# Kernel optimization log

Measured on AMD Instinct MI355X. Metric: run time of the kernel, lower is better.

## Reference

```python
import jax, jax.numpy as jnp
import numpy as np

N_CHANNELS = 512
D_K = 64
N_HEADS = N_CHANNELS // D_K  # 8
SCALE = 1.0 / np.sqrt(np.sqrt(D_K))
EPS = 1e-8


def pixnorm(x, axis=-1):
    return x * jax.lax.rsqrt(jnp.mean(x * x, axis=axis, keepdims=True) + EPS)


def setup_inputs() -> dict:
    key = jax.random.key(0)
    k1, k2, k3 = jax.random.split(key, 3)
    x = jax.random.normal(k1, (16, N_CHANNELS, 32, 32), dtype=jnp.float32)
    # 1x1 conv weights (bias=False) stored as [out, in]
    w_proj = jax.random.normal(k2, (3 * N_CHANNELS, N_CHANNELS), dtype=jnp.float32) * (1.0 / np.sqrt(N_CHANNELS))
    w_out = jax.random.normal(k3, (N_CHANNELS, N_CHANNELS), dtype=jnp.float32) * (1.0 / np.sqrt(N_CHANNELS))
    return {"x": x, "w_proj": w_proj, "w_out": w_out}


def reference(x, w_proj, w_out):
    B, C, H, W = x.shape
    S = H * W
    # tokens: [B, S, C]
    xt = x.reshape(B, C, S).transpose(0, 2, 1)
    # 1x1 conv projection -> [B, S, 3C]
    h = jnp.einsum('bsc,oc->bso', xt, w_proj)
    qkv = h.reshape(B, S, N_HEADS, 3 * D_K)
    q, k, v = jnp.split(qkv, 3, axis=-1)  # each [B, S, H, d]
    q = pixnorm(q)
    k = pixnorm(k)
    v = pixnorm(v)
    attn = jnp.einsum('bihd,bjhd->bijh', q * SCALE, k * SCALE)
    attn = jax.nn.softmax(attn, axis=2)
    res = jnp.einsum('bijh,bjhd->bihd', attn, v)  # [B, S, H, d]
    res = res.reshape(B, S, C)
    res = jnp.einsum('bsc,oc->bso', res, w_out)
    res = res.transpose(0, 2, 1).reshape(B, C, H, W)
    return x + res
```

## Files before the change

### kernel.cpp

```cpp
#include <hip/hip_runtime.h>
#include <hip/hip_bf16.h>
#include <math.h>

typedef float f32x4 __attribute__((ext_vector_type(4)));
typedef __bf16 bf16x8 __attribute__((ext_vector_type(8)));
typedef __bf16 bf16x4 __attribute__((ext_vector_type(4)));
typedef unsigned u32x4 __attribute__((ext_vector_type(4)));

#define DEVFN static __device__ __forceinline__

DEVFN void gload16(const void* g, void* l) {
  __builtin_amdgcn_global_load_lds(
      (const __attribute__((address_space(1))) unsigned int*)g,
      (__attribute__((address_space(3))) unsigned int*)l, 16, 0, 0);
}

DEVFN f32x4 mfma16(bf16x8 a, bf16x8 b, f32x4 c) {
  return __builtin_amdgcn_mfma_f32_16x16x32_bf16(a, b, c, 0, 0, 0);
}

DEVFN unsigned cvtpk(float lo, float hi) {
  unsigned r;
  asm("v_cvt_pk_bf16_f32 %0, %1, %2" : "=v"(r) : "v"(lo), "v"(hi));
  return r;
}

__global__ __launch_bounds__(256) void cast_weights_k(
    const float* __restrict__ wp, const float* __restrict__ wo,
    __bf16* __restrict__ wpb, __bf16* __restrict__ wob) {
  int i = blockIdx.x * 256 + threadIdx.x;
  if (i < 1536 * 512) {
    wpb[i] = (__bf16)wp[i];
  } else {
    int j = i - 1536 * 512;
    wob[j] = (__bf16)wo[j];
  }
}

__global__ __launch_bounds__(256) void transpose_x_k(const float* __restrict__ x,
                                                     __bf16* __restrict__ xt) {
  __shared__ float tile[64][65];
  int b = blockIdx.z, c0 = blockIdx.y * 64, s0 = blockIdx.x * 64;
  int t = threadIdx.x;
  int r = t >> 2, q = (t & 3) << 4;
  const float* src = x + ((size_t)(b * 512 + c0 + r)) * 1024 + s0 + q;
#pragma unroll
  for (int i = 0; i < 4; i++) {
    float4 f = *reinterpret_cast<const float4*>(src + i * 4);
    tile[r][q + i * 4 + 0] = f.x;
    tile[r][q + i * 4 + 1] = f.y;
    tile[r][q + i * 4 + 2] = f.z;
    tile[r][q + i * 4 + 3] = f.w;
  }
  __syncthreads();
  bf16x8 o0, o1;
#pragma unroll
  for (int i = 0; i < 8; i++) o0[i] = (__bf16)tile[q + i][r];
#pragma unroll
  for (int i = 0; i < 8; i++) o1[i] = (__bf16)tile[q + 8 + i][r];
  __bf16* dst = xt + ((size_t)(b * 1024 + s0 + r)) * 512 + c0 + q;
  *reinterpret_cast<bf16x8*>(dst) = o0;
  *reinterpret_cast<bf16x8*>(dst + 8) = o1;
}

template <int MODE>
__global__ __launch_bounds__(256) void gemm_bt_k(
    const __bf16* __restrict__ A, const __bf16* __restrict__ Bt,
    float* __restrict__ Cf, const float* __restrict__ Xres,
    __bf16* __restrict__ Qo, __bf16* __restrict__ Ko, __bf16* __restrict__ Vto,
    int ldc, long bstride_bt, long bstride_c) {
  __shared__ __attribute__((aligned(16))) char smem[32768];
  const int K = 512;
  int n0 = blockIdx.x * 128, m0 = blockIdx.y * 128;
  int z = blockIdx.z;
  Bt += (size_t)z * bstride_bt;
  int tid = threadIdx.x, wave = tid >> 6, lane = tid & 63;
  int fr = lane & 15, fq = lane >> 4;
  int wm = (wave >> 1) * 64, wn = (wave & 1) * 64;
  f32x4 acc[4][4] = {};
  int od[4], ro[4], sp[4];
#pragma unroll
  for (int i = 0; i < 4; i++) {
    od[i] = wave * 4096 + i * 1024 + lane * 16;
    ro[i] = od[i] >> 7;
    sp[i] = (od[i] & 127) ^ ((ro[i] & 7) << 4);
  }
  int rsw = (fr & 7) << 4;
  const char* Ap = (const char*)A;
  const char* Bp = (const char*)Bt;
  for (int k0 = 0; k0 < K; k0 += 64) {
    __syncthreads();
#pragma unroll
    for (int i = 0; i < 4; i++)
      gload16(Ap + (size_t)(m0 + ro[i]) * 1024 + k0 * 2 + sp[i], smem + od[i]);
#pragma unroll
    for (int i = 0; i < 4; i++)
      gload16(Bp + (size_t)(n0 + ro[i]) * 1024 + k0 * 2 + sp[i], smem + 16384 + od[i]);
    __syncthreads();
#pragma unroll
    for (int kk = 0; kk < 2; kk++) {
      bf16x8 af[4], bfr[4];
#pragma unroll
      for (int mi = 0; mi < 4; mi++)
        af[mi] = *reinterpret_cast<const bf16x8*>(
            smem + (wm + mi * 16 + fr) * 128 + ((kk * 64 + fq * 16) ^ rsw));
#pragma unroll
      for (int ni = 0; ni < 4; ni++)
        bfr[ni] = *reinterpret_cast<const bf16x8*>(
            smem + 16384 + (wn + ni * 16 + fr) * 128 + ((kk * 64 + fq * 16) ^ rsw));
      __builtin_amdgcn_s_setprio(1);
#pragma unroll
      for (int mi = 0; mi < 4; mi++)
#pragma unroll
        for (int ni = 0; ni < 4; ni++)
          acc[mi][ni] = mfma16(af[mi], bfr[ni], acc[mi][ni]);
      __builtin_amdgcn_s_setprio(0);
    }
  }
  if (MODE == 1) {
    float* Co = Cf + (size_t)z * bstride_c;
    const float* Xr = Xres + (size_t)z * bstride_c;
#pragma unroll
    for (int mi = 0; mi < 4; mi++)
#pragma unroll
      for (int i = 0; i < 4; i++) {
        int row = m0 + wm + mi * 16 + fq * 4 + i;
#pragma unroll
        for (int ni = 0; ni < 4; ni++) {
          size_t idx = (size_t)row * ldc + n0 + wn + ni * 16 + fr;
          Co[idx] = acc[mi][ni][i] + Xr[idx];
        }
      }
  } else {
    int g0 = n0 + wn;
    int head = g0 / 192;
    int grp = (g0 >> 6) % 3;
    int b = m0 >> 10, sb = m0 & 1023;
    int bh = b * 8 + head;
    float nrm[4][4];
#pragma unroll
    for (int mi = 0; mi < 4; mi++)
#pragma unroll
      for (int i = 0; i < 4; i++) {
        float ss = 0.f;
#pragma unroll
        for (int ni = 0; ni < 4; ni++) ss += acc[mi][ni][i] * acc[mi][ni][i];
#pragma unroll
        for (int off = 1; off < 16; off <<= 1) ss += __shfl_xor(ss, off);
        float nv = rsqrtf(ss * (1.0f / 64.0f) + 1e-8f);
        if (grp == 0) nv *= 0.18033688011112042f;
        nrm[mi][i] = nv;
      }
    if (grp < 2) {
      __bf16* dst = (grp == 0 ? Qo : Ko) + (size_t)bh * 65536;
#pragma unroll
      for (int mi = 0; mi < 4; mi++)
#pragma unroll
        for (int i = 0; i < 4; i++) {
          int s = sb + wm + mi * 16 + fq * 4 + i;
#pragma unroll
          for (int ni = 0; ni < 4; ni++)
            dst[(size_t)s * 64 + ni * 16 + fr] = (__bf16)(acc[mi][ni][i] * nrm[mi][i]);
        }
    }
    __syncthreads();
    if (grp == 2) {
#pragma unroll
      for (int mi = 0; mi < 4; mi++)
#pragma unroll
        for (int i = 0; i < 4; i++) {
          int r = wm + mi * 16 + fq * 4 + i;
#pragma unroll
          for (int ni = 0; ni < 4; ni++) {
            int col2 = (2 * (ni * 16 + fr)) ^ ((r & 31) << 2);
            *(__bf16*)(smem + r * 128 + col2) = (__bf16)(acc[mi][ni][i] * nrm[mi][i]);
          }
        }
    }
    __syncthreads();
    if (grp == 2) {
      int sl = wm + lane;
      int l = sl & 63;
      int pl = ((l >> 2) & 3) * 16 + (l >> 4) * 4 + (l & 3);
      __bf16* vdst = Vto + (size_t)bh * 65536 + sb + (sl & 64) + pl;
#pragma unroll 8
      for (int d = 0; d < 64; d++) {
        __bf16 v = *(const __bf16*)(smem + sl * 128 + ((2 * d) ^ ((sl & 31) << 2)));
        vdst[(size_t)d * 1024] = v;
      }
    }
  }
}

__global__ __launch_bounds__(256, 4) void attn_k(const __bf16* __restrict__ Q,
                                                 const __bf16* __restrict__ Kb,
                                                 const __bf16* __restrict__ Vt,
                                                 __bf16* __restrict__ Res) {
  __shared__ __attribute__((aligned(16))) char lds[32768];
  int p = blockIdx.x;
  int v = (p & 7) * 128 + (p >> 3);
  int qt = v & 7, bh = v >> 3;
  int wave = threadIdx.x >> 6, lane = threadIdx.x & 63;
  int fr = lane & 15, fq = lane >> 4;
  const __bf16* Qb = Q + (size_t)bh * 65536;
  const char* Kbase = (const char*)(Kb + (size_t)bh * 65536);
  const char* Vbase = (const char*)(Vt + (size_t)bh * 65536);
  bf16x8 qf[2][2];
#pragma unroll
  for (int qs = 0; qs < 2; qs++)
#pragma unroll
    for (int kk = 0; kk < 2; kk++)
      qf[qs][kk] = *reinterpret_cast<const bf16x8*>(
          Qb + (size_t)(qt * 128 + qs * 64 + wave * 16 + fr) * 64 + kk * 32 + fq * 8);

  bf16x8 ones;
#pragma unroll
  for (int j = 0; j < 8; j++) ones[j] = (__bf16)1.0f;

  f32x4 oa[2][4] = {};
  f32x4 lacc[2] = {};

  int o0 = wave * 2048 + lane * 16;
  int o1 = o0 + 1024;
  int r0 = o0 >> 7, c0 = o0 & 127, r1 = o1 >> 7, c1 = o1 & 127;
  int s0 = c0 ^ ((r0 & 7) << 4), s1 = c1 ^ ((r1 & 7) << 4);
  int swr = (fr & 7) << 4;

#define STAGE(kt_, buf_)                                                        \
  {                                                                             \
    char* ks_ = lds + (buf_)*8192;                                              \
    char* vs_ = lds + 16384 + (buf_)*8192;                                      \
    gload16(Kbase + (size_t)(kt_)*8192 + r0 * 128 + s0, ks_ + o0);              \
    gload16(Kbase + (size_t)(kt_)*8192 + r1 * 128 + s1, ks_ + o1);              \
    gload16(Vbase + (size_t)r0 * 2048 + (kt_)*128 + s0, vs_ + o0);              \
    gload16(Vbase + (size_t)r1 * 2048 + (kt_)*128 + s1, vs_ + o1);              \
  }

  STAGE(0, 0);
  __syncthreads();
  for (int kt = 0; kt < 16; kt++) {
    int cur = kt & 1;
    if (kt + 1 < 16) STAGE(kt + 1, cur ^ 1);
    const char* ksc = lds + cur * 8192;
    const char* vsc = lds + 16384 + cur * 8192;
    f32x4 sa[2][4] = {};
    __builtin_amdgcn_s_setprio(1);
#pragma unroll
    for (int ni = 0; ni < 4; ni++) {
      bf16x8 kf0 = *reinterpret_cast<const bf16x8*>(
          ksc + (ni * 16 + fr) * 128 + ((fq * 16) ^ swr));
      bf16x8 kf1 = *reinterpret_cast<const bf16x8*>(
          ksc + (ni * 16 + fr) * 128 + ((64 + fq * 16) ^ swr));
#pragma unroll
      for (int qs = 0; qs < 2; qs++) {
        sa[qs][ni] = mfma16(kf0, qf[qs][0], sa[qs][ni]);
        sa[qs][ni] = mfma16(kf1, qf[qs][1], sa[qs][ni]);
      }
    }
    __builtin_amdgcn_s_setprio(0);
    bf16x8 pb[2][2];
#pragma unroll
    for (int qs = 0; qs < 2; qs++) {
#pragma unroll
      for (int ni = 0; ni < 4; ni++)
#pragma unroll
        for (int i = 0; i < 4; i++)
          sa[qs][ni][i] = __builtin_amdgcn_exp2f(sa[qs][ni][i]);
#pragma unroll
      for (int kk2 = 0; kk2 < 2; kk2++) {
        u32x4 u;
        u[0] = cvtpk(sa[qs][2 * kk2][0], sa[qs][2 * kk2][1]);
        u[1] = cvtpk(sa[qs][2 * kk2][2], sa[qs][2 * kk2][3]);
        u[2] = cvtpk(sa[qs][2 * kk2 + 1][0], sa[qs][2 * kk2 + 1][1]);
        u[3] = cvtpk(sa[qs][2 * kk2 + 1][2], sa[qs][2 * kk2 + 1][3]);
        pb[qs][kk2] = __builtin_bit_cast(bf16x8, u);
      }
      lacc[qs] = mfma16(ones, pb[qs][0], lacc[qs]);
      lacc[qs] = mfma16(ones, pb[qs][1], lacc[qs]);
    }
    __builtin_amdgcn_s_setprio(1);
#pragma unroll
    for (int nd = 0; nd < 4; nd++) {
      int vrow = (nd * 16 + fr) * 128;
#pragma unroll
      for (int kk2 = 0; kk2 < 2; kk2++) {
        bf16x8 vf = *reinterpret_cast<const bf16x8*>(
            vsc + vrow + ((fq * 32 + kk2 * 16) ^ swr));
#pragma unroll
        for (int qs = 0; qs < 2; qs++)
          oa[qs][nd] = mfma16(vf, pb[qs][kk2], oa[qs][nd]);
      }
    }
    __builtin_amdgcn_s_setprio(0);
    __syncthreads();
  }
  int b = bh >> 3, hd = bh & 7;
#pragma unroll
  for (int qs = 0; qs < 2; qs++) {
    int q = qt * 128 + qs * 64 + wave * 16 + fr;
    float inv_l = 1.0f / lacc[qs][0];
    __bf16* dst = Res + ((size_t)(b * 1024 + q)) * 512 + hd * 64 + fq * 4;
#pragma unroll
    for (int nd = 0; nd < 4; nd++) {
      bf16x4 ov;
#pragma unroll
      for (int i = 0; i < 4; i++) ov[i] = (__bf16)(oa[qs][nd][i] * inv_l);
      *reinterpret_cast<bf16x4*>(dst + nd * 16) = ov;
    }
  }
#undef STAGE
}

extern "C" void kernel_launch(void* const* d_in, const int* in_sizes, int n_in,
                              void* d_out, int out_size, void* d_ws, size_t ws_size,
                              hipStream_t stream) {
  const float* x = (const float*)d_in[0];
  const float* wp = (const float*)d_in[1];
  const float* wo = (const float*)d_in[2];
  float* out = (float*)d_out;
  char* w = (char*)d_ws;
  __bf16* wpb = (__bf16*)(w);
  __bf16* wob = (__bf16*)(w + 1572864);
  __bf16* xt = (__bf16*)(w + 2097152);
  __bf16* Qb = (__bf16*)(w + 18874368);
  __bf16* Kb = (__bf16*)(w + 35651584);
  __bf16* Vtb = (__bf16*)(w + 52428800);
  __bf16* resb = (__bf16*)(w + 69206016);

  cast_weights_k<<<4096, 256, 0, stream>>>(wp, wo, wpb, wob);
  transpose_x_k<<<dim3(16, 8, 16), 256, 0, stream>>>(x, xt);
  gemm_bt_k<2><<<dim3(12, 128, 1), 256, 0, stream>>>(xt, wpb, nullptr, nullptr,
                                                     Qb, Kb, Vtb, 1536, 0, 0);
  attn_k<<<1024, 256, 0, stream>>>(Qb, Kb, Vtb, resb);
  gemm_bt_k<1><<<dim3(8, 4, 16), 256, 0, stream>>>(wob, resb, out, x,
                                                   nullptr, nullptr, nullptr, 1024,
                                                   1024L * 512, 512L * 1024);
}
```

Measured before the change: 123.9 us.

## Double-buffer GEMM LDS tiles and remap blocks for XCD-local L2 reuse

The projection and output GEMMs now use a two-stage LDS ring with a K-step of 32. The next tile's global-to-LDS loads are issued before the current tile's MFMAs, which leaves one barrier per iteration instead of two. Blocks move to a 1D grid with an XCD-aware mapping, so blocks on the same XCD share A rows (MODE 2) or batch slices (MODE 1) for better L2 locality. The smaller K-step doubles the iteration count, and the swizzle is reworked for 64-byte rows.

```diff
diff --git a/kernel.cpp b/kernel.cpp
--- a/kernel.cpp
+++ b/kernel.cpp
@@ -67,59 +67,80 @@
 __global__ __launch_bounds__(256) void gemm_bt_k(
     const __bf16* __restrict__ A, const __bf16* __restrict__ Bt,
     float* __restrict__ Cf, const float* __restrict__ Xres,
-    __bf16* __restrict__ Qo, __bf16* __restrict__ Ko, __bf16* __restrict__ Vto,
-    int ldc, long bstride_bt, long bstride_c) {
+    __bf16* __restrict__ Qo, __bf16* __restrict__ Ko, __bf16* __restrict__ Vto) {
   __shared__ __attribute__((aligned(16))) char smem[32768];
   const int K = 512;
-  int n0 = blockIdx.x * 128, m0 = blockIdx.y * 128;
-  int z = blockIdx.z;
-  Bt += (size_t)z * bstride_bt;
+  int p = blockIdx.x, xcd = p & 7, idx = p >> 3;
+  int m0, n0, z;
+  if (MODE == 2) {
+    m0 = (xcd * 16 + idx / 12) * 128;
+    n0 = (idx % 12) * 128;
+    z = 0;
+  } else {
+    z = xcd * 2 + idx / 32;
+    int rem = idx % 32;
+    m0 = (rem >> 3) * 128;
+    n0 = (rem & 7) * 128;
+    Bt += (size_t)z * (1024L * 512);
+  }
   int tid = threadIdx.x, wave = tid >> 6, lane = tid & 63;
   int fr = lane & 15, fq = lane >> 4;
   int wm = (wave >> 1) * 64, wn = (wave & 1) * 64;
   f32x4 acc[4][4] = {};
-  int od[4], ro[4], sp[4];
-#pragma unroll
-  for (int i = 0; i < 4; i++) {
-    od[i] = wave * 4096 + i * 1024 + lane * 16;
-    ro[i] = od[i] >> 7;
-    sp[i] = (od[i] & 127) ^ ((ro[i] & 7) << 4);
-  }
-  int rsw = (fr & 7) << 4;
+  int offs[2], rr[2], scc[2];
+#pragma unroll
+  for (int i = 0; i < 2; i++) {
+    offs[i] = wave * 2048 + i * 1024 + lane * 16;
+    rr[i] = offs[i] >> 6;
+    scc[i] = (offs[i] & 63) ^ (((rr[i] ^ (rr[i] >> 2)) & 3) << 4);
+  }
+  int rdsw = (fr ^ (fr >> 2)) & 3;
   const char* Ap = (const char*)A;
   const char* Bp = (const char*)Bt;
-  for (int k0 = 0; k0 < K; k0 += 64) {
+
+#define GSTAGE(k0_, buf_)                                                       \
+  {                                                                             \
+    char* as_ = smem + (buf_)*8192;                                             \
+    char* bs_ = smem + 16384 + (buf_)*8192;                                     \
+    _Pragma("unroll") for (int i = 0; i < 2; i++)                               \
+        gload16(Ap + (size_t)(m0 + rr[i]) * 1024 + (k0_)*2 + scc[i],            \
+                as_ + offs[i]);                                                 \
+    _Pragma("unroll") for (int i = 0; i < 2; i++)                               \
+        gload16(Bp + (size_t)(n0 + rr[i]) * 1024 + (k0_)*2 + scc[i],            \
+                bs_ + offs[i]);                                                 \
+  }
+
+  GSTAGE(0, 0);
+  __syncthreads();
+  int cur = 0;
+  for (int k0 = 0; k0 < K; k0 += 32) {
+    if (k0 + 32 < K) GSTAGE(k0 + 32, cur ^ 1);
+    const char* as = smem + cur * 8192;
+    const char* bs = smem + 16384 + cur * 8192;
+    bf16x8 af[4], bfr[4];
+#pragma unroll
+    for (int mi = 0; mi < 4; mi++)
+      af[mi] = *reinterpret_cast<const bf16x8*>(
+          as + (wm + mi * 16 + fr) * 64 + ((fq ^ rdsw) << 4));
+#pragma unroll
+    for (int ni = 0; ni < 4; ni++)
+      bfr[ni] = *reinterpret_cast<const bf16x8*>(
+          bs + (wn + ni * 16 + fr) * 64 + ((fq ^ rdsw) << 4));
+    __builtin_amdgcn_s_setprio(1);
+#pragma unroll
+    for (int mi = 0; mi < 4; mi++)
+#pragma unroll
+      for (int ni = 0; ni < 4; ni++)
+        acc[mi][ni] = mfma16(af[mi], bfr[ni], acc[mi][ni]);
+    __builtin_amdgcn_s_setprio(0);
     __syncthreads();
-#pragma unroll
-    for (int i = 0; i < 4; i++)
-      gload16(Ap + (size_t)(m0 + ro[i]) * 1024 + k0 * 2 + sp[i], smem + od[i]);
-#pragma unroll
-    for (int i = 0; i < 4; i++)
-      gload16(Bp + (size_t)(n0 + ro[i]) * 1024 + k0 * 2 + sp[i], smem + 16384 + od[i]);
-    __syncthreads();
-#pragma unroll
-    for (int kk = 0; kk < 2; kk++) {
-      bf16x8 af[4], bfr[4];
-#pragma unroll
-      for (int mi = 0; mi < 4; mi++)
-        af[mi] = *reinterpret_cast<const bf16x8*>(
-            smem + (wm + mi * 16 + fr) * 128 + ((kk * 64 + fq * 16) ^ rsw));
-#pragma unroll
-      for (int ni = 0; ni < 4; ni++)
-        bfr[ni] = *reinterpret_cast<const bf16x8*>(
-            smem + 16384 + (wn + ni * 16 + fr) * 128 + ((kk * 64 + fq * 16) ^ rsw));
-      __builtin_amdgcn_s_setprio(1);
-#pragma unroll
-      for (int mi = 0; mi < 4; mi++)
-#pragma unroll
-        for (int ni = 0; ni < 4; ni++)
-          acc[mi][ni] = mfma16(af[mi], bfr[ni], acc[mi][ni]);
-      __builtin_amdgcn_s_setprio(0);
-    }
-  }
+    cur ^= 1;
+  }
+#undef GSTAGE
+
   if (MODE == 1) {
-    float* Co = Cf + (size_t)z * bstride_c;
-    const float* Xr = Xres + (size_t)z * bstride_c;
+    float* Co = Cf + (size_t)z * (512L * 1024);
+    const float* Xr = Xres + (size_t)z * (512L * 1024);
 #pragma unroll
     for (int mi = 0; mi < 4; mi++)
 #pragma unroll
@@ -127,8 +148,8 @@
         int row = m0 + wm + mi * 16 + fq * 4 + i;
 #pragma unroll
         for (int ni = 0; ni < 4; ni++) {
-          size_t idx = (size_t)row * ldc + n0 + wn + ni * 16 + fr;
-          Co[idx] = acc[mi][ni][i] + Xr[idx];
+          size_t idxo = (size_t)row * 1024 + n0 + wn + ni * 16 + fr;
+          Co[idxo] = acc[mi][ni][i] + Xr[idxo];
         }
       }
   } else {
@@ -329,10 +350,8 @@
 
   cast_weights_k<<<4096, 256, 0, stream>>>(wp, wo, wpb, wob);
   transpose_x_k<<<dim3(16, 8, 16), 256, 0, stream>>>(x, xt);
-  gemm_bt_k<2><<<dim3(12, 128, 1), 256, 0, stream>>>(xt, wpb, nullptr, nullptr,
-                                                     Qb, Kb, Vtb, 1536, 0, 0);
+  gemm_bt_k<2><<<1536, 256, 0, stream>>>(xt, wpb, nullptr, nullptr, Qb, Kb, Vtb);
   attn_k<<<1024, 256, 0, stream>>>(Qb, Kb, Vtb, resb);
-  gemm_bt_k<1><<<dim3(8, 4, 16), 256, 0, stream>>>(wob, resb, out, x,
-                                                   nullptr, nullptr, nullptr, 1024,
-                                                   1024L * 512, 512L * 1024);
-}
+  gemm_bt_k<1><<<512, 256, 0, stream>>>(wob, resb, out, x, nullptr, nullptr,
+                                        nullptr);
+}
```

New measurement: 126.2 us. Within noise of the previous version (+1.8%).
